# Optimization experiments

Measured on AMD Instinct MI355X. Metric: run time of the kernel, lower is better.

Reference implementation:

```python
import jax, jax.numpy as jnp
import numpy as np

N, E, D, H, FF = 50000, 800000, 128, 8, 512
DK = D // H
NTYPES = 5
EPS = 1e-5


def setup_inputs() -> dict:
    key = jax.random.key(0)
    ks = jax.random.split(key, 8)
    x = jax.random.normal(ks[0], (N, D), jnp.float32)
    edges = jax.random.randint(ks[1], (2, E), 0, N)
    etype = jax.random.randint(ks[2], (E,), 0, NTYPES)
    masks = etype[None, :] == jnp.arange(NTYPES)[:, None]  # [5, E] bool, exact partition
    s = 1.0 / np.sqrt(D)
    Wk = jax.random.normal(ks[3], (NTYPES, D, D), jnp.float32) * s
    bk = jnp.zeros((NTYPES, D), jnp.float32)
    ln1_g = jnp.ones((D,), jnp.float32)
    ln1_b = jnp.zeros((D,), jnp.float32)
    ln2_g = jnp.ones((D,), jnp.float32)
    ln2_b = jnp.zeros((D,), jnp.float32)
    W1 = jax.random.normal(ks[4], (D, FF), jnp.float32) * s
    b1 = jnp.zeros((FF,), jnp.float32)
    W2 = jax.random.normal(ks[5], (FF, D), jnp.float32) * (1.0 / np.sqrt(FF))
    b2 = jnp.zeros((D,), jnp.float32)
    return {"x": x, "edges": edges, "masks": masks, "Wk": Wk, "bk": bk,
            "ln1_g": ln1_g, "ln1_b": ln1_b, "ln2_g": ln2_g, "ln2_b": ln2_b,
            "W1": W1, "b1": b1, "W2": W2, "b2": b2}


def _layernorm(x, g, b):
    mu = x.mean(-1, keepdims=True)
    var = x.var(-1, keepdims=True)
    return (x - mu) * jax.lax.rsqrt(var + EPS) * g + b


def _proj(z, idx, masks, W, b):
    # per-edge-type masked linear: output[mask_i] = x[idx[mask_i]] @ W_i + b_i
    g = z[idx]  # [E, D] gather
    out = jnp.zeros((g.shape[0], D), z.dtype)
    for i in range(NTYPES):
        out = out + jnp.where(masks[i][:, None], g @ W[i] + b[i], 0.0)
    return out.reshape(-1, H, DK)  # [E, H, d_k]


def reference(x, edges, masks, Wk, bk, ln1_g, ln1_b, ln2_g, ln2_b, W1, b1, W2, b2):
    src, dst = edges[0], edges[1]
    n = x.shape[0]
    z = _layernorm(x, ln1_g, ln1_b)
    # source module uses self.key projection for query, key AND value
    q = _proj(z, src, masks, Wk, bk)   # [E, H, d_k]
    k = _proj(z, dst, masks, Wk, bk)   # [E, H, d_k]
    v = k                              # value = key(z, edges[1]) == key, reuse
    logits = (q * k).sum(2, keepdims=True)  # [E, H, 1], unscaled as in source
    m = jax.ops.segment_max(jax.lax.stop_gradient(logits), src, num_segments=n)
    scores = jnp.exp(logits - m[src])
    den = jax.ops.segment_sum(scores, src, num_segments=n)
    scores = scores / den[src]
    attn = jax.ops.segment_sum(scores * v, src, num_segments=n).reshape(n, -1)  # [N, D]
    x = x + attn
    z2 = _layernorm(x, ln2_g, ln2_b)
    ff = jax.nn.relu(z2 @ W1 + b1) @ W2 + b2
    return x + ff
```

## Files before the change

kernel.cpp:

```cpp
#include <hip/hip_runtime.h>

#define D 128
#define H 8
#define DK 16
#define FFDIM 512
#define NTYPES 5
#define LN_EPS 1e-5f

typedef __bf16 bf16x8 __attribute__((ext_vector_type(8)));
typedef float f32x4 __attribute__((ext_vector_type(4)));
typedef unsigned short ushort_t;
typedef unsigned int uint_t;

__device__ inline ushort_t bfbits(float f) {
  __bf16 b = (__bf16)f;
  return __builtin_bit_cast(ushort_t, b);
}

__global__ void detect_kernel(const unsigned char* __restrict__ m8, int E,
                              int* __restrict__ flag) {
  int lane = threadIdx.x;
  int s = 1;
  if (lane < E) {
    s = 0;
#pragma unroll
    for (int i = 0; i < NTYPES; ++i) s += (m8[(size_t)i * E + lane] != 0);
  }
  unsigned long long b = __ballot(s == 1);
  if (lane == 0) *flag = (b == ~0ull) ? 1 : 0;
}

__device__ inline int decode_etype(const unsigned char* __restrict__ m8,
                                   int E, int e, int is8) {
  int t = 0;
  if (is8) {
#pragma unroll
    for (int i = 1; i < NTYPES; ++i) t += i * (m8[(size_t)i * E + e] != 0);
  } else {
    const int* m32 = (const int*)m8;
#pragma unroll
    for (int i = 1; i < NTYPES; ++i) t += i * (m32[(size_t)i * E + e] != 0);
  }
  return t > (NTYPES - 1) ? (NTYPES - 1) : t;
}

__global__ __launch_bounds__(256) void ln1_kernel(
    const float* __restrict__ x, const float* __restrict__ g,
    const float* __restrict__ b, ushort_t* __restrict__ zh,
    ushort_t* __restrict__ zl, int n) {
  int row = blockIdx.x * 4 + (threadIdx.x >> 6);
  int lane = threadIdx.x & 63;
  if (row >= n) return;
  const float* xr = x + (size_t)row * D;
  float v0 = xr[lane], v1 = xr[lane + 64];
  float s = v0 + v1, ss = v0 * v0 + v1 * v1;
  for (int o = 32; o; o >>= 1) { s += __shfl_xor(s, o); ss += __shfl_xor(ss, o); }
  float mu = s * (1.f / D);
  float var = ss * (1.f / D) - mu * mu;
  float rs = rsqrtf(var + LN_EPS);
  float z0 = (v0 - mu) * rs * g[lane] + b[lane];
  float z1 = (v1 - mu) * rs * g[lane + 64] + b[lane + 64];
  size_t o0 = (size_t)row * D + lane, o1 = o0 + 64;
  __bf16 h0 = (__bf16)z0, h1 = (__bf16)z1;
  zh[o0] = __builtin_bit_cast(ushort_t, h0);
  zh[o1] = __builtin_bit_cast(ushort_t, h1);
  __bf16 l0 = (__bf16)(z0 - (float)h0), l1 = (__bf16)(z1 - (float)h1);
  zl[o0] = __builtin_bit_cast(ushort_t, l0);
  zl[o1] = __builtin_bit_cast(ushort_t, l1);
}

__global__ void conv_frag_kernel(const float* __restrict__ W,
                                 ushort_t* __restrict__ hi,
                                 int K, int Ncol, size_t matW, size_t matF) {
  int gid = blockIdx.x * 256 + threadIdx.x;
  int total = (Ncol / 16) * (K / 32) * 64;
  if (gid >= total) return;
  const float* Wm = W + (size_t)blockIdx.y * matW;
  ushort_t* him = hi + (size_t)blockIdx.y * matF;
  int l = gid & 63;
  int ck = gid >> 6;
  int kk = ck % (K / 32);
  int c = ck / (K / 32);
  int row0 = kk * 32 + (l >> 4) * 8;
  int col = c * 16 + (l & 15);
  size_t ob = (size_t)gid * 8;
#pragma unroll
  for (int j = 0; j < 8; ++j) {
    float w = Wm[(size_t)(row0 + j) * Ncol + col];
    __bf16 h = (__bf16)w;
    him[ob + j] = __builtin_bit_cast(ushort_t, h);
  }
}

__global__ __launch_bounds__(256, 3) void proj_mfma_kernel(
    const ushort_t* __restrict__ zh, const ushort_t* __restrict__ zl,
    const ushort_t* __restrict__ wkh,
    const float* __restrict__ bk, ushort_t* __restrict__ P, int n) {
  int w = threadIdx.x >> 6, l = threadIdx.x & 63;
  int n0 = blockIdx.x * 64 + w * 16;
  int arow = n0 + (l & 15);
  if (arow >= n) arow = n - 1;
  int koff = (l >> 4) * 8;
  bf16x8 ah[4], al[4];
#pragma unroll
  for (int kk = 0; kk < 4; ++kk) {
    size_t zo = (size_t)arow * D + kk * 32 + koff;
    ah[kk] = *(const bf16x8*)(zh + zo);
    al[kk] = *(const bf16x8*)(zl + zo);
  }
  int col16 = l & 15, rgrp = (l >> 4) * 4;
  for (int t = 0; t < NTYPES; ++t) {
    const ushort_t* bh0 = wkh + (size_t)t * (D * D);
    ushort_t* Pt = P + (size_t)t * n * D;
#pragma unroll
    for (int cp = 0; cp < 4; ++cp) {
      bf16x8 Bh[2][4];
#pragma unroll
      for (int cc = 0; cc < 2; ++cc)
#pragma unroll
        for (int kk = 0; kk < 4; ++kk) {
          size_t o = ((size_t)((cp * 2 + cc) * 4 + kk) * 64 + l) * 8;
          Bh[cc][kk] = *(const bf16x8*)(bh0 + o);
        }
      f32x4 aa[2], ac[2];
#pragma unroll
      for (int cc = 0; cc < 2; ++cc) {
        float bias = bk[t * D + (cp * 2 + cc) * 16 + col16];
        aa[cc] = (f32x4){bias, bias, bias, bias};
        ac[cc] = (f32x4){0.f, 0.f, 0.f, 0.f};
      }
#pragma unroll
      for (int kk = 0; kk < 4; ++kk)
#pragma unroll
        for (int cc = 0; cc < 2; ++cc) {
          aa[cc] = __builtin_amdgcn_mfma_f32_16x16x32_bf16(ah[kk], Bh[cc][kk], aa[cc], 0, 0, 0);
          ac[cc] = __builtin_amdgcn_mfma_f32_16x16x32_bf16(al[kk], Bh[cc][kk], ac[cc], 0, 0, 0);
        }
#pragma unroll
      for (int cc = 0; cc < 2; ++cc)
#pragma unroll
        for (int r = 0; r < 4; ++r) {
          int row = n0 + rgrp + r;
          if (row < n)
            Pt[(size_t)row * D + (cp * 2 + cc) * 16 + col16] =
                bfbits(aa[cc][r] + ac[cc][r]);
        }
    }
  }
}

__global__ void zero_kernel(int* __restrict__ p, int n) {
  int i = blockIdx.x * 256 + threadIdx.x;
  if (i < n) p[i] = 0;
}

__global__ void hist5_kernel(const int* __restrict__ edges,
                             const unsigned char* __restrict__ masks,
                             const int* __restrict__ flag,
                             int* __restrict__ cnt5,
                             unsigned char* __restrict__ etype8, int E) {
  int e = blockIdx.x * 256 + threadIdx.x;
  if (e >= E) return;
  int t = decode_etype(masks, E, e, *flag);
  etype8[e] = (unsigned char)t;
  atomicAdd(&cnt5[edges[e] * 8 + t], 1);
}

__global__ __launch_bounds__(256) void scanA5_kernel(const int* __restrict__ cnt5,
                                                     int* __restrict__ loc,
                                                     int* __restrict__ bsums, int n) {
  __shared__ int ts[256];
  int tid = threadIdx.x;
  int i = blockIdx.x * 256 + tid;
  int v = 0;
  if (i < n) {
    int4 c0 = *(const int4*)(cnt5 + (size_t)i * 8);
    v = c0.x + c0.y + c0.z + c0.w + cnt5[(size_t)i * 8 + 4];
  }
  ts[tid] = v;
  __syncthreads();
  for (int o = 1; o < 256; o <<= 1) {
    int t = (tid >= o) ? ts[tid - o] : 0;
    __syncthreads();
    ts[tid] += t;
    __syncthreads();
  }
  if (i < n) loc[i] = ts[tid] - v;
  if (tid == 255) bsums[blockIdx.x] = ts[255];
}

__global__ __launch_bounds__(256) void scanB_kernel(int* __restrict__ bsums, int nb,
                                                    int* __restrict__ total) {
  __shared__ int ts[256];
  int tid = threadIdx.x;
  int per = (nb + 255) / 256;
  int start = tid * per;
  int end = min(start + per, nb);
  int s = 0;
  for (int i = start; i < end; ++i) s += bsums[i];
  ts[tid] = s;
  __syncthreads();
  for (int o = 1; o < 256; o <<= 1) {
    int t = (tid >= o) ? ts[tid - o] : 0;
    __syncthreads();
    ts[tid] += t;
    __syncthreads();
  }
  int run = ts[tid] - s;
  for (int i = start; i < end; ++i) {
    int v = bsums[i];
    bsums[i] = run;
    run += v;
  }
  if (tid == 255) *total = ts[255];
}

__global__ void scanC_kernel(const int* __restrict__ loc,
                             const int* __restrict__ bsums,
                             const int* __restrict__ total,
                             int* __restrict__ offs, int n) {
  int i = blockIdx.x * 256 + threadIdx.x;
  if (i < n) offs[i] = loc[i] + bsums[i >> 8];
  if (i == 0) offs[n] = *total;
}

__global__ void build5_kernel(const int* __restrict__ offs,
                              const int* __restrict__ cnt5,
                              int* __restrict__ cursor5, int* __restrict__ tb,
                              int n) {
  int i = blockIdx.x * 256 + threadIdx.x;
  if (i >= n) return;
  int base = offs[i];
#pragma unroll
  for (int t = 0; t < NTYPES; ++t) {
    int c = cnt5[(size_t)i * 8 + t];
    cursor5[(size_t)i * 8 + t] = base;
    tb[(size_t)i * 8 + t] = base;
    base += c;
  }
  tb[(size_t)i * 8 + 5] = base;
}

__global__ void fill_kernel(const int* __restrict__ edges,
                            const unsigned char* __restrict__ etype8,
                            int* __restrict__ cursor5,
                            int* __restrict__ elist, int E, int n) {
  int e = blockIdx.x * 256 + threadIdx.x;
  if (e >= E) return;
  int t = etype8[e];
  int dst = edges[E + e];
  int pos = atomicAdd(&cursor5[edges[e] * 8 + t], 1);
  elist[pos] = t * n + dst;
}

__global__ __launch_bounds__(256, 4) void attn_kernel(
    const float* __restrict__ x, const ushort_t* __restrict__ P,
    const int* __restrict__ tb, const int* __restrict__ elist,
    float* __restrict__ out, int n) {
  int node = (blockIdx.x * 256 + threadIdx.x) >> 4;
  int gl = threadIdx.x & 15;
  if (node >= n) return;

  int4 t03 = *(const int4*)(tb + (size_t)node * 8);
  int2 t45 = *(const int2*)(tb + (size_t)node * 8 + 4);
  int bnd0 = t03.x, bnd1 = t03.y, bnd2 = t03.z, bnd3 = t03.w;
  int bnd4 = t45.x, bnd5 = t45.y;

  float m = -1e30f, den = 0.f;
  float a[8];
#pragma unroll
  for (int i = 0; i < 8; ++i) a[i] = 0.f;

#pragma unroll
  for (int t = 0; t < NTYPES; ++t) {
    int jb = (t == 0) ? bnd0 : (t == 1) ? bnd1 : (t == 2) ? bnd2
             : (t == 3) ? bnd3 : bnd4;
    int je = (t == 0) ? bnd1 : (t == 1) ? bnd2 : (t == 2) ? bnd3
             : (t == 3) ? bnd4 : bnd5;
    if (jb >= je) continue;
    bf16x8 qb = *(const bf16x8*)(P + (size_t)(t * n + node) * D + gl * 8);
    float qf[8];
#pragma unroll
    for (int d = 0; d < 8; ++d) qf[d] = (float)qb[d];

    int row = elist[jb];
    bf16x8 kv = *(const bf16x8*)(P + (size_t)row * D + gl * 8);
    for (int j = jb; j < je; ++j) {
      bf16x8 kvn = kv;
      if (j + 1 < je) {
        int rn = elist[j + 1];
        kvn = *(const bf16x8*)(P + (size_t)rn * D + gl * 8);
      }
      float kf[8], p = 0.f;
#pragma unroll
      for (int d = 0; d < 8; ++d) {
        kf[d] = (float)kv[d];
        p += qf[d] * kf[d];
      }
      p += __shfl_xor(p, 1);
      float nm = fmaxf(m, p);
      float sc = __expf(m - nm);
      float w = __expf(p - nm);
      den = den * sc + w;
#pragma unroll
      for (int d = 0; d < 8; ++d) a[d] = a[d] * sc + w * kf[d];
      m = nm;
      kv = kvn;
    }
  }

  float inv = (bnd5 > bnd0) ? 1.f / den : 0.f;
  const float* xr = x + (size_t)node * D + gl * 8;
  float* orow = out + (size_t)node * D + gl * 8;
  float4 xa = *(const float4*)xr;
  float4 xb = *(const float4*)(xr + 4);
  float4 oa, ob;
  oa.x = xa.x + a[0] * inv; oa.y = xa.y + a[1] * inv;
  oa.z = xa.z + a[2] * inv; oa.w = xa.w + a[3] * inv;
  ob.x = xb.x + a[4] * inv; ob.y = xb.y + a[5] * inv;
  ob.z = xb.z + a[6] * inv; ob.w = xb.w + a[7] * inv;
  *(float4*)orow = oa;
  *(float4*)(orow + 4) = ob;
}

__global__ __launch_bounds__(256, 3) void ffn_mfma_kernel(
    const ushort_t* __restrict__ w1h, const ushort_t* __restrict__ w2h,
    const float* __restrict__ b1, const float* __restrict__ b2,
    const float* __restrict__ g, const float* __restrict__ bln,
    float* __restrict__ out, int n) {
  __shared__ ushort_t z2h[64 * D];
  __shared__ ushort_t z2l[64 * D];
  __shared__ float hmb[4][16 * 36];
  int tid = threadIdx.x, w = tid >> 6, l = tid & 63;
  int n0 = blockIdx.x * 64;

  for (int i = w; i < 64; i += 4) {
    int r = n0 + i;
    float v0 = 0.f, v1 = 0.f;
    if (r < n) {
      v0 = out[(size_t)r * D + l];
      v1 = out[(size_t)r * D + 64 + l];
    }
    float s = v0 + v1, ss = v0 * v0 + v1 * v1;
    for (int o = 32; o; o >>= 1) { s += __shfl_xor(s, o); ss += __shfl_xor(ss, o); }
    float mu = s * (1.f / D);
    float var = ss * (1.f / D) - mu * mu;
    float rs = rsqrtf(var + LN_EPS);
    float z0 = (v0 - mu) * rs * g[l] + bln[l];
    float z1 = (v1 - mu) * rs * g[l + 64] + bln[l + 64];
    int sw = (i & 7) << 3;
    int e0 = (i * D + l) ^ sw;
    int e1 = (i * D + l + 64) ^ sw;
    __bf16 h0 = (__bf16)z0, h1 = (__bf16)z1;
    z2h[e0] = __builtin_bit_cast(ushort_t, h0);
    z2h[e1] = __builtin_bit_cast(ushort_t, h1);
    __bf16 l0 = (__bf16)(z0 - (float)h0), l1 = (__bf16)(z1 - (float)h1);
    z2l[e0] = __builtin_bit_cast(ushort_t, l0);
    z2l[e1] = __builtin_bit_cast(ushort_t, l1);
  }
  __syncthreads();

  int lrow = w * 16 + (l & 15);
  int koff = (l >> 4) * 8;
  bf16x8 ah[4], al[4];
#pragma unroll
  for (int kk = 0; kk < 4; ++kk) {
    int e = (lrow * D + kk * 32 + koff) ^ ((lrow & 7) << 3);
    ah[kk] = *(const bf16x8*)(z2h + e);
    al[kk] = *(const bf16x8*)(z2l + e);
  }

  int col16 = l & 15, rgrp = (l >> 4) * 4;
  f32x4 acc2[8];
#pragma unroll
  for (int c = 0; c < 8; ++c) acc2[c] = (f32x4){0.f, 0.f, 0.f, 0.f};
  float* hbp = &hmb[w][0];

  for (int kk2 = 0; kk2 < 16; ++kk2) {
    bf16x8 B1h[2][4];
#pragma unroll
    for (int cc = 0; cc < 2; ++cc)
#pragma unroll
      for (int kk = 0; kk < 4; ++kk) {
        size_t o = ((size_t)((kk2 * 2 + cc) * 4 + kk) * 64 + l) * 8;
        B1h[cc][kk] = *(const bf16x8*)(w1h + o);
      }
    f32x4 ha[2], hc[2];
#pragma unroll
    for (int cc = 0; cc < 2; ++cc) {
      float bias = b1[(kk2 * 2 + cc) * 16 + col16];
      ha[cc] = (f32x4){bias, bias, bias, bias};
      hc[cc] = (f32x4){0.f, 0.f, 0.f, 0.f};
    }
#pragma unroll
    for (int kk = 0; kk < 4; ++kk)
#pragma unroll
      for (int cc = 0; cc < 2; ++cc) {
        ha[cc] = __builtin_amdgcn_mfma_f32_16x16x32_bf16(ah[kk], B1h[cc][kk], ha[cc], 0, 0, 0);
        hc[cc] = __builtin_amdgcn_mfma_f32_16x16x32_bf16(al[kk], B1h[cc][kk], hc[cc], 0, 0, 0);
      }
#pragma unroll
    for (int cc = 0; cc < 2; ++cc)
#pragma unroll
      for (int r = 0; r < 4; ++r)
        hbp[(rgrp + r) * 36 + cc * 16 + col16] =
            fmaxf(ha[cc][r] + hc[cc][r], 0.f);
    float av[8];
    *(float4*)&av[0] = *(const float4*)&hbp[(l & 15) * 36 + koff];
    *(float4*)&av[4] = *(const float4*)&hbp[(l & 15) * 36 + koff + 4];
    bf16x8 a2h, a2l;
#pragma unroll
    for (int j = 0; j < 8; ++j) {
      __bf16 hv = (__bf16)av[j];
      a2h[j] = hv;
      a2l[j] = (__bf16)(av[j] - (float)hv);
    }
    bf16x8 B2h[8];
#pragma unroll
    for (int c2 = 0; c2 < 8; ++c2) {
      size_t o = ((size_t)(c2 * 16 + kk2) * 64 + l) * 8;
      B2h[c2] = *(const bf16x8*)(w2h + o);
    }
#pragma unroll
    for (int c2 = 0; c2 < 8; ++c2) {
      acc2[c2] = __builtin_amdgcn_mfma_f32_16x16x32_bf16(a2h, B2h[c2], acc2[c2], 0, 0, 0);
      acc2[c2] = __builtin_amdgcn_mfma_f32_16x16x32_bf16(a2l, B2h[c2], acc2[c2], 0, 0, 0);
    }
  }

#pragma unroll
  for (int c2 = 0; c2 < 8; ++c2) {
    float bias2 = b2[c2 * 16 + col16];
#pragma unroll
    for (int r = 0; r < 4; ++r) {
      int row = n0 + w * 16 + rgrp + r;
      if (row < n) {
        size_t o = (size_t)row * D + c2 * 16 + col16;
        out[o] = out[o] + acc2[c2][r] + bias2;
      }
    }
  }
}

extern "C" void kernel_launch(void* const* d_in, const int* in_sizes, int n_in,
                              void* d_out, int out_size, void* d_ws, size_t ws_size,
                              hipStream_t stream) {
  const float* x      = (const float*)d_in[0];
  const int* edges    = (const int*)d_in[1];
  const unsigned char* masks = (const unsigned char*)d_in[2];
  const float* Wk     = (const float*)d_in[3];
  const float* bk     = (const float*)d_in[4];
  const float* ln1_g  = (const float*)d_in[5];
  const float* ln1_b  = (const float*)d_in[6];
  const float* ln2_g  = (const float*)d_in[7];
  const float* ln2_b  = (const float*)d_in[8];
  const float* W1     = (const float*)d_in[9];
  const float* b1     = (const float*)d_in[10];
  const float* W2     = (const float*)d_in[11];
  const float* b2     = (const float*)d_in[12];
  float* out = (float*)d_out;

  const int n = in_sizes[0] / D;
  const int E = in_sizes[1] / 2;
  const int nbn = (n + 255) / 256;

  char* ws = (char*)d_ws;
  size_t off = 0;
  ushort_t* P = (ushort_t*)(ws + off);  off += (size_t)NTYPES * n * D * sizeof(ushort_t);
  int* cnt5   = (int*)(ws + off);       off += (size_t)n * 8 * sizeof(int);
  int* cursor5= (int*)(ws + off);       off += (size_t)n * 8 * sizeof(int);
  int* tb     = (int*)(ws + off);       off += (size_t)n * 8 * sizeof(int);
  int* offs   = (int*)(ws + off);       off += (size_t)(n + 1) * sizeof(int);
  int* loc    = (int*)(ws + off);       off += (size_t)n * sizeof(int);
  int* bsums  = (int*)(ws + off);       off += (size_t)nbn * sizeof(int);
  int* total  = (int*)(ws + off);       off += 64;
  int* elist  = (int*)(ws + off);       off += (size_t)E * sizeof(int);
  unsigned char* etype8 = (unsigned char*)(ws + off); off += (size_t)E + 64;
  int* flag   = (int*)(ws + off);       off += 64;
  ushort_t* wkh = (ushort_t*)(ws + off); off += (size_t)NTYPES * D * D * sizeof(ushort_t);
  ushort_t* w1h = (ushort_t*)(ws + off); off += (size_t)D * FFDIM * sizeof(ushort_t);
  ushort_t* w2h = (ushort_t*)(ws + off); off += (size_t)FFDIM * D * sizeof(ushort_t);
  (void)ws_size; (void)n_in; (void)out_size;

  ushort_t* zh = (ushort_t*)out;
  ushort_t* zl = zh + (size_t)n * D;

  detect_kernel<<<1, 64, 0, stream>>>(masks, E, flag);

  ln1_kernel<<<(n + 3) / 4, 256, 0, stream>>>(x, ln1_g, ln1_b, zh, zl, n);

  {
    dim3 gwk((8 * 4 * 64 + 255) / 256, NTYPES);
    conv_frag_kernel<<<gwk, 256, 0, stream>>>(Wk, wkh, D, D,
                                              (size_t)D * D, (size_t)D * D);
    dim3 gw1(((FFDIM / 16) * 4 * 64 + 255) / 256, 1);
    conv_frag_kernel<<<gw1, 256, 0, stream>>>(W1, w1h, D, FFDIM, 0, 0);
    dim3 gw2((8 * (FFDIM / 32) * 64 + 255) / 256, 1);
    conv_frag_kernel<<<gw2, 256, 0, stream>>>(W2, w2h, FFDIM, D, 0, 0);
  }

  proj_mfma_kernel<<<(n + 63) / 64, 256, 0, stream>>>(zh, zl, wkh, bk, P, n);

  zero_kernel<<<(n * 8 + 255) / 256, 256, 0, stream>>>(cnt5, n * 8);
  hist5_kernel<<<(E + 255) / 256, 256, 0, stream>>>(edges, masks, flag, cnt5, etype8, E);
  scanA5_kernel<<<nbn, 256, 0, stream>>>(cnt5, loc, bsums, n);
  scanB_kernel<<<1, 256, 0, stream>>>(bsums, nbn, total);
  scanC_kernel<<<(n + 255) / 256, 256, 0, stream>>>(loc, bsums, total, offs, n);
  build5_kernel<<<(n + 255) / 256, 256, 0, stream>>>(offs, cnt5, cursor5, tb, n);
  fill_kernel<<<(E + 255) / 256, 256, 0, stream>>>(edges, etype8, cursor5, elist, E, n);

  attn_kernel<<<(n + 15) / 16, 256, 0, stream>>>(x, P, tb, elist, out, n);

  ffn_mfma_kernel<<<(n + 63) / 64, 256, 0, stream>>>(w1h, w2h,
                                                     b1, b2, ln2_g, ln2_b, out, n);
}
```

Measured before the change: 278.5 us.

## Split FFN tile across wave pairs to halve per-wave accumulators

The FFN kernel now handles 32 rows per block instead of 64. Each pair of waves shares a 16-row slice, and each wave computes half of the hidden columns in the first GEMM and half of the output columns in the second. The hidden activations are exchanged through a double-buffered shared tile with a block barrier every step. This halves accumulator and weight-fragment registers so the launch bound can rise to 4 blocks per SIMD. The cost is a sync per iteration and each weight fragment being loaded for half as many rows.

Result: faster. 261.2 us (-6.2%).

```diff
diff --git a/kernel.cpp b/kernel.cpp
--- a/kernel.cpp
+++ b/kernel.cpp
@@ -323,18 +323,19 @@
   *(float4*)(orow + 4) = ob;
 }
 
-__global__ __launch_bounds__(256, 3) void ffn_mfma_kernel(
+__global__ __launch_bounds__(256, 4) void ffn_mfma_kernel(
     const ushort_t* __restrict__ w1h, const ushort_t* __restrict__ w2h,
     const float* __restrict__ b1, const float* __restrict__ b2,
     const float* __restrict__ g, const float* __restrict__ bln,
     float* __restrict__ out, int n) {
-  __shared__ ushort_t z2h[64 * D];
-  __shared__ ushort_t z2l[64 * D];
-  __shared__ float hmb[4][16 * 36];
+  __shared__ ushort_t z2h[32 * D];
+  __shared__ ushort_t z2l[32 * D];
+  __shared__ float hb2[2][2][16 * 36];
   int tid = threadIdx.x, w = tid >> 6, l = tid & 63;
-  int n0 = blockIdx.x * 64;
-
-  for (int i = w; i < 64; i += 4) {
+  int n0 = blockIdx.x * 32;
+  int r2 = w >> 1, c2h = w & 1;
+
+  for (int i = w; i < 32; i += 4) {
     int r = n0 + i;
     float v0 = 0.f, v1 = 0.f;
     if (r < n) {
@@ -360,7 +361,7 @@
   }
   __syncthreads();
 
-  int lrow = w * 16 + (l & 15);
+  int lrow = r2 * 16 + (l & 15);
   int koff = (l >> 4) * 8;
   bf16x8 ah[4], al[4];
 #pragma unroll
@@ -371,43 +372,35 @@
   }
 
   int col16 = l & 15, rgrp = (l >> 4) * 4;
-  f32x4 acc2[8];
-#pragma unroll
-  for (int c = 0; c < 8; ++c) acc2[c] = (f32x4){0.f, 0.f, 0.f, 0.f};
-  float* hbp = &hmb[w][0];
+  f32x4 acc2[4];
+#pragma unroll
+  for (int c = 0; c < 4; ++c) acc2[c] = (f32x4){0.f, 0.f, 0.f, 0.f};
 
   for (int kk2 = 0; kk2 < 16; ++kk2) {
-    bf16x8 B1h[2][4];
-#pragma unroll
-    for (int cc = 0; cc < 2; ++cc)
-#pragma unroll
-      for (int kk = 0; kk < 4; ++kk) {
-        size_t o = ((size_t)((kk2 * 2 + cc) * 4 + kk) * 64 + l) * 8;
-        B1h[cc][kk] = *(const bf16x8*)(w1h + o);
-      }
-    f32x4 ha[2], hc[2];
-#pragma unroll
-    for (int cc = 0; cc < 2; ++cc) {
-      float bias = b1[(kk2 * 2 + cc) * 16 + col16];
-      ha[cc] = (f32x4){bias, bias, bias, bias};
-      hc[cc] = (f32x4){0.f, 0.f, 0.f, 0.f};
-    }
-#pragma unroll
-    for (int kk = 0; kk < 4; ++kk)
-#pragma unroll
-      for (int cc = 0; cc < 2; ++cc) {
-        ha[cc] = __builtin_amdgcn_mfma_f32_16x16x32_bf16(ah[kk], B1h[cc][kk], ha[cc], 0, 0, 0);
-        hc[cc] = __builtin_amdgcn_mfma_f32_16x16x32_bf16(al[kk], B1h[cc][kk], hc[cc], 0, 0, 0);
-      }
-#pragma unroll
-    for (int cc = 0; cc < 2; ++cc)
-#pragma unroll
-      for (int r = 0; r < 4; ++r)
-        hbp[(rgrp + r) * 36 + cc * 16 + col16] =
-            fmaxf(ha[cc][r] + hc[cc][r], 0.f);
+    int c = kk2 * 2 + c2h;
+    bf16x8 B1h[4];
+#pragma unroll
+    for (int kk = 0; kk < 4; ++kk) {
+      size_t o = ((size_t)(c * 4 + kk) * 64 + l) * 8;
+      B1h[kk] = *(const bf16x8*)(w1h + o);
+    }
+    float bias = b1[c * 16 + col16];
+    f32x4 ha = {bias, bias, bias, bias};
+    f32x4 hc = {0.f, 0.f, 0.f, 0.f};
+#pragma unroll
+    for (int kk = 0; kk < 4; ++kk) {
+      ha = __builtin_amdgcn_mfma_f32_16x16x32_bf16(ah[kk], B1h[kk], ha, 0, 0, 0);
+      hc = __builtin_amdgcn_mfma_f32_16x16x32_bf16(al[kk], B1h[kk], hc, 0, 0, 0);
+    }
+    float* hbp = &hb2[kk2 & 1][r2][0];
+#pragma unroll
+    for (int r = 0; r < 4; ++r)
+      hbp[(rgrp + r) * 36 + c2h * 16 + col16] = fmaxf(ha[r] + hc[r], 0.f);
+    __syncthreads();
     float av[8];
-    *(float4*)&av[0] = *(const float4*)&hbp[(l & 15) * 36 + koff];
-    *(float4*)&av[4] = *(const float4*)&hbp[(l & 15) * 36 + koff + 4];
+    const float* hbr = &hb2[kk2 & 1][r2][0];
+    *(float4*)&av[0] = *(const float4*)&hbr[(l & 15) * 36 + koff];
+    *(float4*)&av[4] = *(const float4*)&hbr[(l & 15) * 36 + koff + 4];
     bf16x8 a2h, a2l;
 #pragma unroll
     for (int j = 0; j < 8; ++j) {
@@ -415,28 +408,30 @@
       a2h[j] = hv;
       a2l[j] = (__bf16)(av[j] - (float)hv);
     }
-    bf16x8 B2h[8];
-#pragma unroll
-    for (int c2 = 0; c2 < 8; ++c2) {
-      size_t o = ((size_t)(c2 * 16 + kk2) * 64 + l) * 8;
-      B2h[c2] = *(const bf16x8*)(w2h + o);
-    }
-#pragma unroll
-    for (int c2 = 0; c2 < 8; ++c2) {
-      acc2[c2] = __builtin_amdgcn_mfma_f32_16x16x32_bf16(a2h, B2h[c2], acc2[c2], 0, 0, 0);
-      acc2[c2] = __builtin_amdgcn_mfma_f32_16x16x32_bf16(a2l, B2h[c2], acc2[c2], 0, 0, 0);
-    }
-  }
-
-#pragma unroll
-  for (int c2 = 0; c2 < 8; ++c2) {
-    float bias2 = b2[c2 * 16 + col16];
+    bf16x8 B2h[4];
+#pragma unroll
+    for (int cc2 = 0; cc2 < 4; ++cc2) {
+      int ct = c2h * 4 + cc2;
+      size_t o = ((size_t)(ct * 16 + kk2) * 64 + l) * 8;
+      B2h[cc2] = *(const bf16x8*)(w2h + o);
+    }
+#pragma unroll
+    for (int cc2 = 0; cc2 < 4; ++cc2) {
+      acc2[cc2] = __builtin_amdgcn_mfma_f32_16x16x32_bf16(a2h, B2h[cc2], acc2[cc2], 0, 0, 0);
+      acc2[cc2] = __builtin_amdgcn_mfma_f32_16x16x32_bf16(a2l, B2h[cc2], acc2[cc2], 0, 0, 0);
+    }
+  }
+
+#pragma unroll
+  for (int cc2 = 0; cc2 < 4; ++cc2) {
+    int col = (c2h * 4 + cc2) * 16 + col16;
+    float bias2 = b2[col];
 #pragma unroll
     for (int r = 0; r < 4; ++r) {
-      int row = n0 + w * 16 + rgrp + r;
+      int row = n0 + r2 * 16 + rgrp + r;
       if (row < n) {
-        size_t o = (size_t)row * D + c2 * 16 + col16;
-        out[o] = out[o] + acc2[c2][r] + bias2;
+        size_t o = (size_t)row * D + col;
+        out[o] = out[o] + acc2[cc2][r] + bias2;
       }
     }
   }
@@ -511,6 +506,6 @@
 
   attn_kernel<<<(n + 15) / 16, 256, 0, stream>>>(x, P, tb, elist, out, n);
 
-  ffn_mfma_kernel<<<(n + 63) / 64, 256, 0, stream>>>(w1h, w2h,
+  ffn_mfma_kernel<<<(n + 31) / 32, 256, 0, stream>>>(w1h, w2h,
                                                      b1, b2, ln2_g, ln2_b, out, n);
 }
```
